# Kernel tuning notes

Measured on AMD Instinct MI355X. Metric: run time of the kernel, lower is better.

The kernel has to match this reference:

```python
import jax, jax.numpy as jnp
import numpy as np

B, S, D, H = 4, 2048, 1024, 16
HD = D // H
SCALE = float(np.sqrt(HD))

def setup_inputs() -> dict:
    key = jax.random.key(0)
    ks = jax.random.split(key, 6)
    std = 1.0 / np.sqrt(D)
    return {
        "x": jax.random.normal(ks[0], (B, S, D), dtype=jnp.float32),
        "Wq": jax.random.normal(ks[1], (D, D), dtype=jnp.float32) * std,
        "Wk": jax.random.normal(ks[2], (D, D), dtype=jnp.float32) * std,
        "Wv": jax.random.normal(ks[3], (D, D), dtype=jnp.float32) * std,
        "Wo": jax.random.normal(ks[4], (D, D), dtype=jnp.float32) * std,
        "bo": jnp.zeros((D,), dtype=jnp.float32),
    }

def reference(x, Wq, Wk, Wv, Wo, bo):
    b, s, _ = x.shape
    # nn.Linear(y) = y @ W.T ; project then split heads -> [B,H,S,HD]
    def proj(W):
        return (x @ W.T).reshape(b, s, H, HD).transpose(0, 2, 1, 3)
    q, k, v = proj(Wq), proj(Wk), proj(Wv)
    scores = jnp.einsum("bhqd,bhkd->bhqk", q, k) / SCALE
    causal = jnp.triu(jnp.ones((s, s), dtype=bool), k=1)
    scores = jnp.where(causal[None, None, :, :], -jnp.inf, scores)
    attn = jax.nn.softmax(scores, axis=-1)  # dropout is identity in eval mode
    out = jnp.einsum("bhqk,bhkd->bhqd", attn, v)
    out = out.transpose(0, 2, 1, 3).reshape(b, s, D)
    return out @ Wo.T + bo
```

## Files before the change

### kernel.cpp

```cpp
#include <hip/hip_runtime.h>
#include <hip/hip_bf16.h>

constexpr int Sc = 2048, Dc = 1024;

typedef __attribute__((ext_vector_type(8))) short bf16x8;
typedef __attribute__((ext_vector_type(4))) short short4v;
typedef __attribute__((ext_vector_type(4))) float f32x4;
typedef __attribute__((ext_vector_type(16))) float f32x16;

static __device__ __forceinline__ short f2bf(float f) {
  __hip_bfloat16 h = __float2bfloat16(f);
  short s; __builtin_memcpy(&s, &h, 2);
  return s;
}

static __device__ __forceinline__ unsigned int cvtpk(float lo, float hi) {
  unsigned int r;
  asm("v_cvt_pk_bf16_f32 %0, %1, %2" : "=v"(r) : "v"(lo), "v"(hi));
  return r;
}

typedef __attribute__((address_space(3))) short lds_short_t;

static __device__ __forceinline__ void gload16(const short* g, lds_short_t* l) {
  __builtin_amdgcn_global_load_lds(
      (const __attribute__((address_space(1))) unsigned int*)g,
      (__attribute__((address_space(3))) unsigned int*)l, 16, 0, 0);
}

__global__ __launch_bounds__(256) void cvt_f32_bf16(const float* __restrict__ src,
                                                    short* __restrict__ dst,
                                                    int n4) {
  int i = blockIdx.x * 256 + threadIdx.x;
  if (i >= n4) return;
  float4 v = ((const float4*)src)[i];
  short4v o;
  o.x = f2bf(v.x); o.y = f2bf(v.y); o.z = f2bf(v.z); o.w = f2bf(v.w);
  ((short4v*)dst)[i] = o;
}

__global__ __launch_bounds__(256) void cvt_w4(const float* __restrict__ w0,
                                              const float* __restrict__ w1,
                                              const float* __restrict__ w2,
                                              const float* __restrict__ w3,
                                              short* __restrict__ dst) {
  const int y = blockIdx.y;
  const float* src = (y == 0) ? w0 : (y == 1) ? w1 : (y == 2) ? w2 : w3;
  int i = blockIdx.x * 256 + threadIdx.x;
  float4 v = ((const float4*)src)[i];
  short4v o;
  o.x = f2bf(v.x); o.y = f2bf(v.y); o.z = f2bf(v.z); o.w = f2bf(v.w);
  ((short4v*)(dst))[(size_t)y * 262144 + i] = o;
}

template <int MODE>
__global__ __launch_bounds__(256) void gemm_db(
    const short* __restrict__ A, const short* __restrict__ W,
    const float* __restrict__ bias, short* __restrict__ Qb,
    short* __restrict__ Kb, short* __restrict__ Vt, float* __restrict__ outF) {
  __shared__ short As[2][128 * 64];
  __shared__ short Bs[2][128 * 64];
  const int tid = threadIdx.x;
  const int m0 = blockIdx.x * 128, n0 = blockIdx.y * 128;
  const int lane = tid & 63, w = tid >> 6;
  const int wr = w >> 1, wc = w & 1;
  const int ll = lane & 15, lh = lane >> 4;

  lds_short_t* As3 = (lds_short_t*)&As[0][0];
  lds_short_t* Bs3 = (lds_short_t*)&Bs[0][0];

  const short* Abase[4];
  const short* Wbase[4];
  int dstOff[4];
#pragma unroll
  for (int i = 0; i < 4; ++i) {
    int slot = i * 256 + tid;
    int row = slot >> 3;
    int gp = (slot & 7) ^ (row & 7);
    Abase[i] = A + (size_t)(m0 + row) * 1024 + gp * 8;
    Wbase[i] = W + (size_t)(n0 + row) * 1024 + gp * 8;
    dstOff[i] = (i * 256 + w * 64) * 8;
  }

  f32x4 acc[4][4] = {};

#pragma unroll
  for (int i = 0; i < 4; ++i) gload16(Abase[i], As3 + dstOff[i]);
#pragma unroll
  for (int i = 0; i < 4; ++i) gload16(Wbase[i], Bs3 + dstOff[i]);
  int cur = 0;

  for (int k0 = 0; k0 < 1024; k0 += 64) {
    __syncthreads();
    if (k0 < 960) {
      int nb = (cur ^ 1) * 8192;
#pragma unroll
      for (int i = 0; i < 4; ++i) gload16(Abase[i] + k0 + 64, As3 + nb + dstOff[i]);
#pragma unroll
      for (int i = 0; i < 4; ++i) gload16(Wbase[i] + k0 + 64, Bs3 + nb + dstOff[i]);
    }

    bf16x8 fa[4][2], fb[4][2];
#pragma unroll
    for (int mi = 0; mi < 4; ++mi) {
      int r = wr * 64 + mi * 16 + ll;
#pragma unroll
      for (int kh = 0; kh < 2; ++kh)
        fa[mi][kh] =
            *(const bf16x8*)&As[cur][r * 64 + (((kh * 4 + lh) ^ (ll & 7)) * 8)];
    }
#pragma unroll
    for (int ni = 0; ni < 4; ++ni) {
      int r = wc * 64 + ni * 16 + ll;
#pragma unroll
      for (int kh = 0; kh < 2; ++kh)
        fb[ni][kh] =
            *(const bf16x8*)&Bs[cur][r * 64 + (((kh * 4 + lh) ^ (ll & 7)) * 8)];
    }
    __builtin_amdgcn_s_setprio(1);
#pragma unroll
    for (int mi = 0; mi < 4; ++mi)
#pragma unroll
      for (int ni = 0; ni < 4; ++ni)
#pragma unroll
        for (int kh = 0; kh < 2; ++kh)
          acc[mi][ni] = __builtin_amdgcn_mfma_f32_16x16x32_bf16(
              fa[mi][kh], fb[ni][kh], acc[mi][ni], 0, 0, 0);
    __builtin_amdgcn_s_setprio(0);
    cur ^= 1;
  }

#pragma unroll
  for (int mi = 0; mi < 4; ++mi) {
#pragma unroll
    for (int ni = 0; ni < 4; ++ni) {
#pragma unroll
      for (int r = 0; r < 4; ++r) {
        int row = m0 + wr * 64 + mi * 16 + lh * 4 + r;
        int n = n0 + wc * 64 + ni * 16 + ll;
        float v = acc[mi][ni][r];
        if constexpr (MODE == 1) {
          outF[(size_t)row * 1024 + n] = v + bias[n];
        } else {
          if (n < 1024) {
            Qb[(size_t)row * 1024 + n] = f2bf(v * 0.18033688f);
          } else if (n < 2048) {
            Kb[(size_t)row * 1024 + (n - 1024)] = f2bf(v);
          } else {
            int cc = n - 2048, hh = cc >> 6, dd = cc & 63;
            int bb = row >> 11, ss = row & 2047;
            Vt[(size_t)((bb * 16 + hh) * 64 + dd) * 2048 + ss] = f2bf(v);
          }
        }
      }
    }
  }
}

__global__ __launch_bounds__(256, 4) void attn_v9(const short* __restrict__ Q,
                                                  const short* __restrict__ K,
                                                  const short* __restrict__ Vt,
                                                  short* __restrict__ AO) {
  __shared__ short Ks[2][64 * 64];
  __shared__ short Vs[2][64 * 64];
  const int tid = threadIdx.x, lane = tid & 63, w = tid >> 6;
  const int l31 = lane & 31, lh2 = lane >> 5;
  const int id = blockIdx.x;
  const int bh = id & 63;
  const int qs = id >> 6;
  const int jj = qs >> 2;
  const int qb = (jj == 0) ? qs : (jj == 1) ? 19 - qs : (jj == 2) ? qs - 4 : 23 - qs;
  const int b = bh >> 4, h = bh & 15;
  const int q0 = qb * 128;
  const int R = q0 + w * 32;
  const int kw_last = (R + 31) >> 6;
  const int kb_max = (q0 + 127) >> 6;
  const short* Qp = Q + (size_t)b * Sc * Dc + h * 64;
  const short* Kp = K + (size_t)b * Sc * Dc + h * 64;
  const short* Vp = Vt + (size_t)bh * 64 * Sc;

  lds_short_t* Ks3 = (lds_short_t*)Ks;
  lds_short_t* Vs3 = (lds_short_t*)Vs;

  bf16x8 qf[4];
#pragma unroll
  for (int dk = 0; dk < 4; ++dk)
    qf[dk] = *(const bf16x8*)&Qp[(size_t)(R + l31) * Dc + dk * 16 + lh2 * 8];

  const short* Kst[2];
  const short* Vst[2];
  int ldsOff[2];
#pragma unroll
  for (int i = 0; i < 2; ++i) {
    int slot = i * 256 + w * 64 + lane;
    int row = slot >> 3;
    int col = ((slot & 7) ^ (row & 7)) * 8;
    Kst[i] = Kp + (size_t)row * 1024 + col;
    Vst[i] = Vp + (size_t)row * 2048 + col;
    ldsOff[i] = (i * 256 + w * 64) * 8;
  }

  f32x16 o0 = {}, o1 = {};
  float lrun = 0.f;

#pragma unroll
  for (int i = 0; i < 2; ++i) {
    gload16(Kst[i], Ks3 + ldsOff[i]);
    gload16(Vst[i], Vs3 + ldsOff[i]);
  }
  int cur = 0;

  for (int kb = 0; kb <= kb_max; ++kb) {
    __syncthreads();
    if (kb < kb_max) {
      int nb = cur ^ 1;
#pragma unroll
      for (int i = 0; i < 2; ++i) {
        gload16(Kst[i] + (size_t)(kb + 1) * 65536, Ks3 + nb * 4096 + ldsOff[i]);
        gload16(Vst[i] + (kb + 1) * 64, Vs3 + nb * 4096 + ldsOff[i]);
      }
    }

    if (kb <= kw_last) {
      const bool diag = (kb == kw_last);
      const bool skipHi = diag && ((R & 63) == 0);

      f32x16 sv0 = {}, sv1 = {};
      {
        const int row = l31, rx = row & 7;
#pragma unroll
        for (int dk = 0; dk < 4; ++dk) {
          bf16x8 kf =
              *(const bf16x8*)&Ks[cur][row * 64 + (((dk * 2 + lh2) ^ rx) * 8)];
          sv0 = __builtin_amdgcn_mfma_f32_32x32x16_bf16(kf, qf[dk], sv0, 0, 0, 0);
        }
      }
      if (!skipHi) {
        const int row = 32 + l31, rx = row & 7;
#pragma unroll
        for (int dk = 0; dk < 4; ++dk) {
          bf16x8 kf =
              *(const bf16x8*)&Ks[cur][row * 64 + (((dk * 2 + lh2) ^ rx) * 8)];
          sv1 = __builtin_amdgcn_mfma_f32_32x32x16_bf16(kf, qf[dk], sv1, 0, 0, 0);
        }
      }

      float ts = 0.f;
      if (!diag) {
#pragma unroll
        for (int r = 0; r < 16; ++r) {
          float e0 = exp2f(sv0[r]);
          float e1 = exp2f(sv1[r]);
          sv0[r] = e0; sv1[r] = e1;
          ts += e0 + e1;
        }
      } else if (skipHi) {
#pragma unroll
        for (int r = 0; r < 16; ++r) {
          int kl = (r & 3) + 8 * (r >> 2) + 4 * lh2;
          float e = (kl > l31) ? 0.f : exp2f(sv0[r]);
          sv0[r] = e;
          ts += e;
        }
      } else {
#pragma unroll
        for (int r = 0; r < 16; ++r) {
          float e = exp2f(sv0[r]);
          sv0[r] = e;
          ts += e;
        }
#pragma unroll
        for (int r = 0; r < 16; ++r) {
          int kl = (r & 3) + 8 * (r >> 2) + 4 * lh2;
          float e = (kl > l31) ? 0.f : exp2f(sv1[r]);
          sv1[r] = e;
          ts += e;
        }
      }
      lrun += ts;

      short4v pa[8];
#pragma unroll
      for (int t = 0; t < 4; ++t) {
        union { unsigned int u[2]; short4v s; } pk;
        pk.u[0] = cvtpk(sv0[4 * t + 0], sv0[4 * t + 1]);
        pk.u[1] = cvtpk(sv0[4 * t + 2], sv0[4 * t + 3]);
        pa[t] = pk.s;
      }
      if (skipHi) {
        const int r0 = l31, rx0 = r0 & 7;
        const int r1 = 32 + l31, rx1 = r1 & 7;
#pragma unroll
        for (int t = 0; t < 4; ++t) {
          short4v vb0 =
              *(const short4v*)&Vs[cur][r0 * 64 + ((t ^ rx0) * 8) + lh2 * 4];
          o0 = __builtin_amdgcn_mfma_f32_32x32x8bf16_1k(pa[t], vb0, o0, 0, 0, 0);
          short4v vb1 =
              *(const short4v*)&Vs[cur][r1 * 64 + ((t ^ rx1) * 8) + lh2 * 4];
          o1 = __builtin_amdgcn_mfma_f32_32x32x8bf16_1k(pa[t], vb1, o1, 0, 0, 0);
        }
      } else {
#pragma unroll
        for (int t = 0; t < 4; ++t) {
          union { unsigned int u[2]; short4v s; } pk;
          pk.u[0] = cvtpk(sv1[4 * t + 0], sv1[4 * t + 1]);
          pk.u[1] = cvtpk(sv1[4 * t + 2], sv1[4 * t + 3]);
          pa[4 + t] = pk.s;
        }
        const int r0 = l31, rx0 = r0 & 7;
        const int r1 = 32 + l31, rx1 = r1 & 7;
#pragma unroll
        for (int t = 0; t < 8; ++t) {
          short4v vb0 =
              *(const short4v*)&Vs[cur][r0 * 64 + ((t ^ rx0) * 8) + lh2 * 4];
          o0 = __builtin_amdgcn_mfma_f32_32x32x8bf16_1k(pa[t], vb0, o0, 0, 0, 0);
        }
#pragma unroll
        for (int t = 0; t < 8; ++t) {
          short4v vb1 =
              *(const short4v*)&Vs[cur][r1 * 64 + ((t ^ rx1) * 8) + lh2 * 4];
          o1 = __builtin_amdgcn_mfma_f32_32x32x8bf16_1k(pa[t], vb1, o1, 0, 0, 0);
        }
      }
    }
    cur ^= 1;
  }

  float ltot = lrun + __shfl_xor(lrun, 32);
#pragma unroll
  for (int r = 0; r < 16; ++r) {
    int qr = (r & 3) + 8 * (r >> 2) + 4 * lh2;
    float lq = __shfl(ltot, qr);
    float inv = 1.0f / lq;
    int rowg = R + qr;
    AO[((size_t)(b * Sc + rowg)) * Dc + h * 64 + l31] = f2bf(o0[r] * inv);
    AO[((size_t)(b * Sc + rowg)) * Dc + h * 64 + 32 + l31] = f2bf(o1[r] * inv);
  }
}

extern "C" void kernel_launch(void* const* d_in, const int* in_sizes, int n_in,
                              void* d_out, int out_size, void* d_ws,
                              size_t ws_size, hipStream_t stream) {
  const float* x = (const float*)d_in[0];
  const float* Wq = (const float*)d_in[1];
  const float* Wk = (const float*)d_in[2];
  const float* Wv = (const float*)d_in[3];
  const float* Wo = (const float*)d_in[4];
  const float* bo = (const float*)d_in[5];
  float* out = (float*)d_out;

  short* Qb = (short*)d_out;
  short* Kb = Qb + (size_t)8192 * 1024;
  short* xb = (short*)d_ws;
  short* AOb = xb;
  short* Wc = xb + (size_t)8192 * 1024;
  short* Vt = Wc + (size_t)4096 * 1024;

  dim3 blk(256);
  hipLaunchKernelGGL(cvt_f32_bf16, dim3(8192), blk, 0, stream, x, xb, 2097152);
  hipLaunchKernelGGL(cvt_w4, dim3(1024, 4), blk, 0, stream, Wq, Wk, Wv, Wo, Wc);

  hipLaunchKernelGGL((gemm_db<0>), dim3(64, 24), blk, 0, stream, xb, Wc,
                     (const float*)nullptr, Qb, Kb, Vt, (float*)nullptr);

  hipLaunchKernelGGL(attn_v9, dim3(1024), blk, 0, stream, Qb, Kb, Vt, AOb);

  hipLaunchKernelGGL((gemm_db<1>), dim3(64, 8), blk, 0, stream, AOb,
                     Wc + (size_t)3072 * 1024, bo, (short*)nullptr,
                     (short*)nullptr, (short*)nullptr, out);
}
```

Baseline: 180.2 us.

## Software-pipeline attention QK^T with softmax/PV across tiles using triple-buffered LDS

Restructures the attention loop so each iteration issues the QK^T MFMAs for the current key tile while running exp, bf16 packing and PV MFMAs for the previous tile. LDS K/V buffers go from two to three so the previous tile's V stays resident while the next tile loads. Launch bounds drop to 3 waves per SIMD to make room for the extra score registers. The aim is to overlap exp/VALU work with matrix-core work, at the cost of lower occupancy and higher register and LDS pressure.

```diff
diff --git a/kernel.cpp b/kernel.cpp
--- a/kernel.cpp
+++ b/kernel.cpp
@@ -157,12 +157,12 @@
   }
 }
 
-__global__ __launch_bounds__(256, 4) void attn_v9(const short* __restrict__ Q,
-                                                  const short* __restrict__ K,
-                                                  const short* __restrict__ Vt,
-                                                  short* __restrict__ AO) {
-  __shared__ short Ks[2][64 * 64];
-  __shared__ short Vs[2][64 * 64];
+__global__ __launch_bounds__(256, 3) void attn_v12(const short* __restrict__ Q,
+                                                   const short* __restrict__ K,
+                                                   const short* __restrict__ Vt,
+                                                   short* __restrict__ AO) {
+  __shared__ short Ks[3][64 * 64];
+  __shared__ short Vs[3][64 * 64];
   const int tid = threadIdx.x, lane = tid & 63, w = tid >> 6;
   const int l31 = lane & 31, lh2 = lane >> 5;
   const int id = blockIdx.x;
@@ -202,129 +202,139 @@
 
   f32x16 o0 = {}, o1 = {};
   float lrun = 0.f;
+  f32x16 svPA = {}, svPB = {}, svNA = {}, svNB = {};
+
+  auto qkTile = [&](int j, int ck, f32x16& s0, f32x16& s1) {
+    const bool skipHi = (j == kw_last) && ((R & 63) == 0);
+#pragma unroll
+    for (int r = 0; r < 16; ++r) { s0[r] = 0.f; s1[r] = 0.f; }
+    {
+      const int row = l31, rx = row & 7;
+#pragma unroll
+      for (int dk = 0; dk < 4; ++dk) {
+        bf16x8 kf =
+            *(const bf16x8*)&Ks[ck][row * 64 + (((dk * 2 + lh2) ^ rx) * 8)];
+        s0 = __builtin_amdgcn_mfma_f32_32x32x16_bf16(kf, qf[dk], s0, 0, 0, 0);
+      }
+    }
+    if (!skipHi) {
+      const int row = 32 + l31, rx = row & 7;
+#pragma unroll
+      for (int dk = 0; dk < 4; ++dk) {
+        bf16x8 kf =
+            *(const bf16x8*)&Ks[ck][row * 64 + (((dk * 2 + lh2) ^ rx) * 8)];
+        s1 = __builtin_amdgcn_mfma_f32_32x32x16_bf16(kf, qf[dk], s1, 0, 0, 0);
+      }
+    }
+  };
+
+  auto finishTile = [&](int j, int cv, f32x16& s0, f32x16& s1) {
+    const bool diag = (j == kw_last);
+    const bool skipHi = diag && ((R & 63) == 0);
+
+    float ts = 0.f;
+    if (!diag) {
+#pragma unroll
+      for (int r = 0; r < 16; ++r) {
+        float e0 = exp2f(s0[r]);
+        float e1 = exp2f(s1[r]);
+        s0[r] = e0; s1[r] = e1;
+        ts += e0 + e1;
+      }
+    } else if (skipHi) {
+#pragma unroll
+      for (int r = 0; r < 16; ++r) {
+        int kl = (r & 3) + 8 * (r >> 2) + 4 * lh2;
+        float e = (kl > l31) ? 0.f : exp2f(s0[r]);
+        s0[r] = e;
+        ts += e;
+      }
+    } else {
+#pragma unroll
+      for (int r = 0; r < 16; ++r) {
+        float e = exp2f(s0[r]);
+        s0[r] = e;
+        ts += e;
+      }
+#pragma unroll
+      for (int r = 0; r < 16; ++r) {
+        int kl = (r & 3) + 8 * (r >> 2) + 4 * lh2;
+        float e = (kl > l31) ? 0.f : exp2f(s1[r]);
+        s1[r] = e;
+        ts += e;
+      }
+    }
+    lrun += ts;
+
+    short4v pa[8];
+#pragma unroll
+    for (int t = 0; t < 4; ++t) {
+      union { unsigned int u[2]; short4v s4; } pk;
+      pk.u[0] = cvtpk(s0[4 * t + 0], s0[4 * t + 1]);
+      pk.u[1] = cvtpk(s0[4 * t + 2], s0[4 * t + 3]);
+      pa[t] = pk.s4;
+    }
+    if (skipHi) {
+      const int r0 = l31, rx0 = r0 & 7;
+      const int r1 = 32 + l31, rx1 = r1 & 7;
+#pragma unroll
+      for (int t = 0; t < 4; ++t) {
+        short4v vb0 =
+            *(const short4v*)&Vs[cv][r0 * 64 + ((t ^ rx0) * 8) + lh2 * 4];
+        o0 = __builtin_amdgcn_mfma_f32_32x32x8bf16_1k(pa[t], vb0, o0, 0, 0, 0);
+        short4v vb1 =
+            *(const short4v*)&Vs[cv][r1 * 64 + ((t ^ rx1) * 8) + lh2 * 4];
+        o1 = __builtin_amdgcn_mfma_f32_32x32x8bf16_1k(pa[t], vb1, o1, 0, 0, 0);
+      }
+    } else {
+#pragma unroll
+      for (int t = 0; t < 4; ++t) {
+        union { unsigned int u[2]; short4v s4; } pk;
+        pk.u[0] = cvtpk(s1[4 * t + 0], s1[4 * t + 1]);
+        pk.u[1] = cvtpk(s1[4 * t + 2], s1[4 * t + 3]);
+        pa[4 + t] = pk.s4;
+      }
+      const int r0 = l31, rx0 = r0 & 7;
+      const int r1 = 32 + l31, rx1 = r1 & 7;
+#pragma unroll
+      for (int t = 0; t < 8; ++t) {
+        short4v vb0 =
+            *(const short4v*)&Vs[cv][r0 * 64 + ((t ^ rx0) * 8) + lh2 * 4];
+        o0 = __builtin_amdgcn_mfma_f32_32x32x8bf16_1k(pa[t], vb0, o0, 0, 0, 0);
+      }
+#pragma unroll
+      for (int t = 0; t < 8; ++t) {
+        short4v vb1 =
+            *(const short4v*)&Vs[cv][r1 * 64 + ((t ^ rx1) * 8) + lh2 * 4];
+        o1 = __builtin_amdgcn_mfma_f32_32x32x8bf16_1k(pa[t], vb1, o1, 0, 0, 0);
+      }
+    }
+  };
 
 #pragma unroll
   for (int i = 0; i < 2; ++i) {
     gload16(Kst[i], Ks3 + ldsOff[i]);
     gload16(Vst[i], Vs3 + ldsOff[i]);
   }
-  int cur = 0;
+  int cc = 0, cn = 1, cp = 2;
 
   for (int kb = 0; kb <= kb_max; ++kb) {
     __syncthreads();
     if (kb < kb_max) {
-      int nb = cur ^ 1;
 #pragma unroll
       for (int i = 0; i < 2; ++i) {
-        gload16(Kst[i] + (size_t)(kb + 1) * 65536, Ks3 + nb * 4096 + ldsOff[i]);
-        gload16(Vst[i] + (kb + 1) * 64, Vs3 + nb * 4096 + ldsOff[i]);
-      }
-    }
-
-    if (kb <= kw_last) {
-      const bool diag = (kb == kw_last);
-      const bool skipHi = diag && ((R & 63) == 0);
-
-      f32x16 sv0 = {}, sv1 = {};
-      {
-        const int row = l31, rx = row & 7;
-#pragma unroll
-        for (int dk = 0; dk < 4; ++dk) {
-          bf16x8 kf =
-              *(const bf16x8*)&Ks[cur][row * 64 + (((dk * 2 + lh2) ^ rx) * 8)];
-          sv0 = __builtin_amdgcn_mfma_f32_32x32x16_bf16(kf, qf[dk], sv0, 0, 0, 0);
-        }
-      }
-      if (!skipHi) {
-        const int row = 32 + l31, rx = row & 7;
-#pragma unroll
-        for (int dk = 0; dk < 4; ++dk) {
-          bf16x8 kf =
-              *(const bf16x8*)&Ks[cur][row * 64 + (((dk * 2 + lh2) ^ rx) * 8)];
-          sv1 = __builtin_amdgcn_mfma_f32_32x32x16_bf16(kf, qf[dk], sv1, 0, 0, 0);
-        }
-      }
-
-      float ts = 0.f;
-      if (!diag) {
-#pragma unroll
-        for (int r = 0; r < 16; ++r) {
-          float e0 = exp2f(sv0[r]);
-          float e1 = exp2f(sv1[r]);
-          sv0[r] = e0; sv1[r] = e1;
-          ts += e0 + e1;
-        }
-      } else if (skipHi) {
-#pragma unroll
-        for (int r = 0; r < 16; ++r) {
-          int kl = (r & 3) + 8 * (r >> 2) + 4 * lh2;
-          float e = (kl > l31) ? 0.f : exp2f(sv0[r]);
-          sv0[r] = e;
-          ts += e;
-        }
-      } else {
-#pragma unroll
-        for (int r = 0; r < 16; ++r) {
-          float e = exp2f(sv0[r]);
-          sv0[r] = e;
-          ts += e;
-        }
-#pragma unroll
-        for (int r = 0; r < 16; ++r) {
-          int kl = (r & 3) + 8 * (r >> 2) + 4 * lh2;
-          float e = (kl > l31) ? 0.f : exp2f(sv1[r]);
-          sv1[r] = e;
-          ts += e;
-        }
-      }
-      lrun += ts;
-
-      short4v pa[8];
-#pragma unroll
-      for (int t = 0; t < 4; ++t) {
-        union { unsigned int u[2]; short4v s; } pk;
-        pk.u[0] = cvtpk(sv0[4 * t + 0], sv0[4 * t + 1]);
-        pk.u[1] = cvtpk(sv0[4 * t + 2], sv0[4 * t + 3]);
-        pa[t] = pk.s;
-      }
-      if (skipHi) {
-        const int r0 = l31, rx0 = r0 & 7;
-        const int r1 = 32 + l31, rx1 = r1 & 7;
-#pragma unroll
-        for (int t = 0; t < 4; ++t) {
-          short4v vb0 =
-              *(const short4v*)&Vs[cur][r0 * 64 + ((t ^ rx0) * 8) + lh2 * 4];
-          o0 = __builtin_amdgcn_mfma_f32_32x32x8bf16_1k(pa[t], vb0, o0, 0, 0, 0);
-          short4v vb1 =
-              *(const short4v*)&Vs[cur][r1 * 64 + ((t ^ rx1) * 8) + lh2 * 4];
-          o1 = __builtin_amdgcn_mfma_f32_32x32x8bf16_1k(pa[t], vb1, o1, 0, 0, 0);
-        }
-      } else {
-#pragma unroll
-        for (int t = 0; t < 4; ++t) {
-          union { unsigned int u[2]; short4v s; } pk;
-          pk.u[0] = cvtpk(sv1[4 * t + 0], sv1[4 * t + 1]);
-          pk.u[1] = cvtpk(sv1[4 * t + 2], sv1[4 * t + 3]);
-          pa[4 + t] = pk.s;
-        }
-        const int r0 = l31, rx0 = r0 & 7;
-        const int r1 = 32 + l31, rx1 = r1 & 7;
-#pragma unroll
-        for (int t = 0; t < 8; ++t) {
-          short4v vb0 =
-              *(const short4v*)&Vs[cur][r0 * 64 + ((t ^ rx0) * 8) + lh2 * 4];
-          o0 = __builtin_amdgcn_mfma_f32_32x32x8bf16_1k(pa[t], vb0, o0, 0, 0, 0);
-        }
-#pragma unroll
-        for (int t = 0; t < 8; ++t) {
-          short4v vb1 =
-              *(const short4v*)&Vs[cur][r1 * 64 + ((t ^ rx1) * 8) + lh2 * 4];
-          o1 = __builtin_amdgcn_mfma_f32_32x32x8bf16_1k(pa[t], vb1, o1, 0, 0, 0);
-        }
-      }
-    }
-    cur ^= 1;
-  }
+        gload16(Kst[i] + (size_t)(kb + 1) * 65536, Ks3 + cn * 4096 + ldsOff[i]);
+        gload16(Vst[i] + (kb + 1) * 64, Vs3 + cn * 4096 + ldsOff[i]);
+      }
+    }
+
+    if (kb <= kw_last) qkTile(kb, cc, svNA, svNB);
+    if (kb >= 1 && (kb - 1) <= kw_last) finishTile(kb - 1, cp, svPA, svPB);
+    if (kb <= kw_last) { svPA = svNA; svPB = svNB; }
+
+    int t = cp; cp = cc; cc = cn; cn = t;
+  }
+  if (kw_last == kb_max) finishTile(kb_max, kb_max % 3, svPA, svPB);
 
   float ltot = lrun + __shfl_xor(lrun, 32);
 #pragma unroll
@@ -363,7 +373,7 @@
   hipLaunchKernelGGL((gemm_db<0>), dim3(64, 24), blk, 0, stream, xb, Wc,
                      (const float*)nullptr, Qb, Kb, Vt, (float*)nullptr);
 
-  hipLaunchKernelGGL(attn_v9, dim3(1024), blk, 0, stream, Qb, Kb, Vt, AOb);
+  hipLaunchKernelGGL(attn_v12, dim3(1024), blk, 0, stream, Qb, Kb, Vt, AOb);
 
   hipLaunchKernelGGL((gemm_db<1>), dim3(64, 8), blk, 0, stream, AOb,
                      Wc + (size_t)3072 * 1024, bo, (short*)nullptr,
```

After: 253.8 us. 1.41x slower.
